# Kernel optimization log

Measured on AMD Instinct MI355X. Metric: run time of the kernel, lower is better.

## Reference

```python
import jax, jax.numpy as jnp
import numpy as np

HIDDEN = 96
INF = 1e30


def setup_inputs() -> dict:
    key = jax.random.key(0)
    ks = jax.random.split(key, 9)
    B, JX, JM, D_IN, D_MEM = 8, 2048, 2048, 150, 150
    GATED = D_IN + D_MEM  # 300
    inputs = jax.random.normal(ks[0], (B, JX, D_IN), dtype=jnp.float32)
    memory = jax.random.normal(ks[1], (B, JM, D_MEM), dtype=jnp.float32)
    mask = jax.random.randint(ks[2], (B, JM), 0, 2, dtype=jnp.int32)
    s_in = 1.0 / np.sqrt(D_IN)
    s_g = 1.0 / np.sqrt(GATED)
    Wi = jax.random.uniform(ks[3], (D_IN, HIDDEN), jnp.float32, -s_in, s_in)
    bi = jax.random.uniform(ks[4], (HIDDEN,), jnp.float32, -s_in, s_in)
    Wm = jax.random.uniform(ks[5], (D_MEM, HIDDEN), jnp.float32, -s_in, s_in)
    bm = jax.random.uniform(ks[6], (HIDDEN,), jnp.float32, -s_in, s_in)
    Wg = jax.random.uniform(ks[7], (GATED, GATED), jnp.float32, -s_g, s_g)
    bg = jax.random.uniform(ks[8], (GATED,), jnp.float32, -s_g, s_g)
    return {"inputs": inputs, "memory": memory, "mask": mask,
            "Wi": Wi, "bi": bi, "Wm": Wm, "bm": bm, "Wg": Wg, "bg": bg}


def reference(inputs, memory, mask, Wi, bi, Wm, bm, Wg, bg):
    # ReLU projections (inference mode: dropout is identity)
    inputs_ = jax.nn.relu(jnp.einsum('bxd,dh->bxh', inputs, Wi) + bi)  # [B,JX,H]
    memory_ = jax.nn.relu(jnp.einsum('byd,dh->byh', memory, Wm) + bm)  # [B,JM,H]
    # Scaled dot-product scores [B,JX,JM]
    scores = jnp.einsum('bxh,byh->bxy', inputs_, memory_) / jnp.sqrt(
        jnp.asarray(HIDDEN, inputs.dtype))
    # Additive mask: -INF where mask==0 (broadcast over JX)
    maskf = mask.astype(inputs.dtype)[:, None, :]  # [B,1,JM]
    scores = scores - INF * (1.0 - maskf)
    logits = jax.nn.softmax(scores, axis=-1)
    outputs = jnp.einsum('bxy,byd->bxd', logits, memory)  # [B,JX,D_MEM]
    res = jnp.concatenate([inputs, outputs], axis=2)  # [B,JX,GATED]
    gate = jax.nn.sigmoid(jnp.einsum('bxg,gk->bxk', res, Wg) + bg)
    return gate * res
```

## Files before the change

### kernel.cpp

```cpp
#include <hip/hip_runtime.h>

#define BB 8
#define JX 2048
#define JMDIM 2048
#define DID 150
#define HID 96
#define GATED 300
#define NSPLIT 4
#define NROWS (BB * JX)

typedef unsigned short u16;
typedef __attribute__((ext_vector_type(8))) short bh8;
typedef __attribute__((ext_vector_type(4))) float f32x4;

#define SCALE2    (0.14724444f)
#define MASK_NEG2 (-1.4426950e30f)

__device__ inline float b2f(u16 u) {
    union { unsigned int i; float f; } c; c.i = ((unsigned int)u) << 16; return c.f;
}
__device__ inline u16 f2b(float f) {
    unsigned int u = __float_as_uint(f);
    unsigned int r = (u + 0x7fffu + ((u >> 16) & 1u)) >> 16;
    return (u16)r;
}

__global__ void prep_kernel(const float* __restrict__ Wi, const float* __restrict__ Wm,
                            const float* __restrict__ Wg,
                            u16* __restrict__ Wti, u16* __restrict__ Wtm,
                            u16* __restrict__ Wgt) {
    int tid = blockIdx.x * blockDim.x + threadIdx.x;
    int nthr = gridDim.x * blockDim.x;
    for (int e = tid; e < 96 * 168; e += nthr) {
        int h = e / 168, d = e - h * 168;
        Wti[e] = (d < DID) ? f2b(Wi[d * HID + h]) : (u16)0;
        Wtm[e] = (d < DID) ? f2b(Wm[d * HID + h]) : (u16)0;
    }
    for (int e = tid; e < 304 * 328; e += nthr) {
        int k = e / 328, d = e - k * 328;
        Wgt[e] = (k < GATED && d < GATED) ? f2b(Wg[d * GATED + k]) : (u16)0;
    }
}

__global__ __launch_bounds__(256) void proj2_kernel(
    const float* __restrict__ inputs, const float* __restrict__ memory,
    const u16* __restrict__ Wti, const u16* __restrict__ Wtm,
    const float* __restrict__ bi, const float* __restrict__ bm,
    u16* __restrict__ Qp, u16* __restrict__ Kp,
    u16* __restrict__ Xi, u16* __restrict__ Vt) {
    __shared__ __align__(16) u16 Xl[64 * 168];
    __shared__ __align__(16) u16 Wl[96 * 168];
    const float *X, *bias; const u16* Wt; u16* Y;
    if (blockIdx.y == 0) { X = inputs; Wt = Wti; bias = bi; Y = Qp; }
    else                 { X = memory; Wt = Wtm; bias = bm; Y = Kp; }
    int tid = threadIdx.x;
    size_t row0 = (size_t)blockIdx.x * 64;

    const float4* Xv = (const float4*)(X + row0 * DID);
    for (int i = tid; i < 2400; i += 256) {
        float4 v = Xv[i];
        int base = i * 4;
#pragma unroll
        for (int k = 0; k < 4; ++k) {
            int idx = base + k;
            int r = idx / DID, d = idx - r * DID;
            Xl[r * 168 + d] = f2b(((const float*)&v)[k]);
        }
    }
    for (int e = tid; e < 64 * 18; e += 256) {
        int r = e / 18, d = 150 + (e - r * 18);
        Xl[r * 168 + d] = 0;
    }
    for (int i = tid; i < 96 * 21; i += 256) {
        *(bh8*)(Wl + i * 8) = *(const bh8*)(Wt + i * 8);
    }
    __syncthreads();

    if (blockIdx.y == 0) {
        for (int e = tid; e < 64 * 20; e += 256) {
            int r = e / 20, c = e - r * 20;
            *(bh8*)(Xi + (row0 + r) * 160 + c * 8) = *(const bh8*)(Xl + r * 168 + c * 8);
        }
    } else {
        int b = blockIdx.x >> 5, jm0 = (blockIdx.x & 31) * 64;
        for (int e = tid; e < 160 * 64; e += 256) {
            int d = e >> 6, c = e & 63;
            u16 v = (d == DID) ? (u16)0x3F80 : Xl[c * 168 + d];
            Vt[((size_t)b * 160 + d) * JMDIM + jm0 + c] = v;
        }
    }

    int wave = tid >> 6, lane = tid & 63, quad = lane >> 4, l15 = lane & 15;
    bh8 af[5];
#pragma unroll
    for (int kc = 0; kc < 5; ++kc)
        af[kc] = *(const bh8*)(Xl + (wave * 16 + l15) * 168 + kc * 32 + quad * 8);
#pragma unroll
    for (int nt = 0; nt < 6; ++nt) {
        f32x4 acc = {0.f, 0.f, 0.f, 0.f};
#pragma unroll
        for (int kc = 0; kc < 5; ++kc) {
            bh8 bf = *(const bh8*)(Wl + (nt * 16 + l15) * 168 + kc * 32 + quad * 8);
            acc = __builtin_amdgcn_mfma_f32_16x16x32_bf16(af[kc], bf, acc, 0, 0, 0);
        }
        int h = nt * 16 + l15;
        float bv = bias[h];
#pragma unroll
        for (int j = 0; j < 4; ++j) {
            float y = acc[j] + bv;
            y = y > 0.f ? y : 0.f;
            Y[(row0 + wave * 16 + quad * 4 + j) * HID + h] = f2b(y);
        }
    }
}

template <int SPLIT>
__global__ __launch_bounds__(256, 2) void attn_kernel(
    const u16* __restrict__ Qp, const u16* __restrict__ Kp,
    const u16* __restrict__ Vt, const int* __restrict__ mask,
    u16* __restrict__ Opart, float* __restrict__ lpart) {
    __shared__ __align__(16) u16 Kl[64 * 104];
    __shared__ __align__(16) u16 Vl[160 * 72];
    __shared__ __align__(16) u16 Pl[128 * 72];
    __shared__ float Ml[64];
    const int b = blockIdx.y;
    const int x0 = blockIdx.x * 128;
    const int tid = threadIdx.x;
    const int wave = tid >> 6, lane = tid & 63;
    const int quad = lane >> 4, l15 = lane & 15;

    bh8 qf[2][3];
#pragma unroll
    for (int mt = 0; mt < 2; ++mt) {
        const u16* qb = Qp + ((size_t)b * JX + x0 + wave * 32 + mt * 16 + l15) * HID + quad * 8;
        qf[mt][0] = *(const bh8*)(qb);
        qf[mt][1] = *(const bh8*)(qb + 32);
        qf[mt][2] = *(const bh8*)(qb + 64);
    }

    f32x4 o[2][10];
    const f32x4 zero4 = {0.f, 0.f, 0.f, 0.f};
#pragma unroll
    for (int mt = 0; mt < 2; ++mt)
#pragma unroll
        for (int i = 0; i < 10; ++i) o[mt][i] = zero4;

    const int nIter = 32 / SPLIT;
    const int jm0_0 = blockIdx.z * nIter * 64;

    const u16* kptr[3]; u16* kdst[3];
#pragma unroll
    for (int t = 0; t < 3; ++t) {
        int i = tid + t * 256, r = i / 12, c = i - r * 12;
        kptr[t] = Kp + ((size_t)b * JMDIM + jm0_0 + r) * HID + c * 8;
        kdst[t] = Kl + r * 104 + c * 8;
    }
    const u16* vptr[5]; u16* vdst[5];
#pragma unroll
    for (int t = 0; t < 5; ++t) {
        int i = tid + t * 256, d = i >> 3, c = i & 7;
        vptr[t] = Vt + ((size_t)b * 160 + d) * JMDIM + jm0_0 + c * 8;
        vdst[t] = Vl + d * 72 + c * 8;
    }
    const int* mptr = mask + b * JMDIM + jm0_0 + (tid & 63);

    bh8 kreg[3], vreg[5]; int mreg = 0;
#pragma unroll
    for (int t = 0; t < 3; ++t) { kreg[t] = *(const bh8*)kptr[t]; kptr[t] += 64 * HID; }
#pragma unroll
    for (int t = 0; t < 5; ++t) { vreg[t] = *(const bh8*)vptr[t]; vptr[t] += 64; }
    if (tid < 64) { mreg = *mptr; mptr += 64; }

    for (int it = 0; it < nIter; ++it) {
        __syncthreads();
#pragma unroll
        for (int t = 0; t < 3; ++t) *(bh8*)kdst[t] = kreg[t];
#pragma unroll
        for (int t = 0; t < 5; ++t) *(bh8*)vdst[t] = vreg[t];
        if (tid < 64) Ml[tid] = mreg ? 0.f : MASK_NEG2;
        if (it + 1 < nIter) {
#pragma unroll
            for (int t = 0; t < 3; ++t) { kreg[t] = *(const bh8*)kptr[t]; kptr[t] += 64 * HID; }
#pragma unroll
            for (int t = 0; t < 5; ++t) { vreg[t] = *(const bh8*)vptr[t]; vptr[t] += 64; }
            if (tid < 64) { mreg = *mptr; mptr += 64; }
        }
        __syncthreads();

        f32x4 s[2][4];
#pragma unroll
        for (int mt = 0; mt < 2; ++mt)
#pragma unroll
            for (int nt = 0; nt < 4; ++nt) s[mt][nt] = zero4;
#pragma unroll
        for (int nt = 0; nt < 4; ++nt) {
#pragma unroll
            for (int kc = 0; kc < 3; ++kc) {
                bh8 bf = *(const bh8*)(Kl + (nt * 16 + l15) * 104 + kc * 32 + quad * 8);
                s[0][nt] = __builtin_amdgcn_mfma_f32_16x16x32_bf16(qf[0][kc], bf, s[0][nt], 0, 0, 0);
                s[1][nt] = __builtin_amdgcn_mfma_f32_16x16x32_bf16(qf[1][kc], bf, s[1][nt], 0, 0, 0);
            }
        }
#pragma unroll
        for (int nt = 0; nt < 4; ++nt) {
            float madd = Ml[nt * 16 + l15];
#pragma unroll
            for (int mt = 0; mt < 2; ++mt)
#pragma unroll
                for (int j = 0; j < 4; ++j) {
                    float p = exp2f(s[mt][nt][j] * SCALE2 + madd);
                    Pl[(wave * 32 + mt * 16 + quad * 4 + j) * 72 + nt * 16 + l15] = f2b(p);
                }
        }
        __threadfence_block();

        bh8 pf[2][2];
#pragma unroll
        for (int mt = 0; mt < 2; ++mt) {
            pf[mt][0] = *(const bh8*)(Pl + (wave * 32 + mt * 16 + l15) * 72 + quad * 8);
            pf[mt][1] = *(const bh8*)(Pl + (wave * 32 + mt * 16 + l15) * 72 + 32 + quad * 8);
        }
#pragma unroll
        for (int nt = 0; nt < 10; ++nt) {
#pragma unroll
            for (int kc = 0; kc < 2; ++kc) {
                bh8 bf = *(const bh8*)(Vl + (nt * 16 + l15) * 72 + kc * 32 + quad * 8);
                o[0][nt] = __builtin_amdgcn_mfma_f32_16x16x32_bf16(pf[0][kc], bf, o[0][nt], 0, 0, 0);
                o[1][nt] = __builtin_amdgcn_mfma_f32_16x16x32_bf16(pf[1][kc], bf, o[1][nt], 0, 0, 0);
            }
        }
    }

    const size_t z = blockIdx.z;
    const int srcLane = (lane & 48) | 6;
#pragma unroll
    for (int mt = 0; mt < 2; ++mt) {
        float lv[4], inv[4];
#pragma unroll
        for (int j = 0; j < 4; ++j) {
            lv[j] = __shfl(o[mt][9][j], srcLane, 64);
            inv[j] = (lv[j] > 0.f) ? 1.f / lv[j] : 0.f;
        }
        size_t grow = (size_t)b * JX + x0 + wave * 32 + mt * 16;
#pragma unroll
        for (int nt = 0; nt < 10; ++nt) {
            int d = nt * 16 + l15;
            if (d < 152) {
#pragma unroll
                for (int j = 0; j < 4; ++j)
                    Opart[(z * NROWS + grow + quad * 4 + j) * 152 + d] = f2b(o[mt][nt][j] * inv[j]);
            }
        }
        if (l15 == 0) {
#pragma unroll
            for (int j = 0; j < 4; ++j)
                lpart[z * NROWS + grow + quad * 4 + j] = lv[j];
        }
    }
}

template <int SPLIT>
__global__ __launch_bounds__(256) void gate_kernel(
    const u16* __restrict__ Xi, const u16* __restrict__ Opart,
    const float* __restrict__ lpart,
    const u16* __restrict__ Wgt, const float* __restrict__ bg,
    float* __restrict__ out) {
    __shared__ __align__(16) u16 Rl[16 * 328];
    __shared__ float Cw[SPLIT * 16];
    int tid = threadIdx.x;
    size_t row0 = (size_t)blockIdx.x * 16;

    if (tid < 16) {
        float l[SPLIT], L = 0.f;
#pragma unroll
        for (int s = 0; s < SPLIT; ++s) {
            l[s] = lpart[(size_t)s * NROWS + row0 + tid];
            L += l[s];
        }
        float invL = (L > 0.f) ? 1.f / L : 0.f;
#pragma unroll
        for (int s = 0; s < SPLIT; ++s) Cw[s * 16 + tid] = l[s] * invL;
    }
    for (int e = tid; e < 16 * 20; e += 256) {
        int r = e / 20, c = e - r * 20;
        *(bh8*)(Rl + r * 328 + c * 8) = *(const bh8*)(Xi + (row0 + r) * 160 + c * 8);
    }
    __syncthreads();
    for (int e = tid; e < 16 * 19; e += 256) {
        int r = e / 19, q = e - r * 19;
        float acc[8];
#pragma unroll
        for (int k = 0; k < 8; ++k) acc[k] = 0.f;
#pragma unroll
        for (int s = 0; s < SPLIT; ++s) {
            bh8 v = *(const bh8*)(Opart + ((size_t)s * NROWS + row0 + r) * 152 + q * 8);
            float w = Cw[s * 16 + r];
#pragma unroll
            for (int k = 0; k < 8; ++k) acc[k] += b2f(((const u16*)&v)[k]) * w;
        }
        u16* dst = Rl + r * 328 + 150 + q * 8;
#pragma unroll
        for (int k = 0; k < 8; ++k) dst[k] = f2b(acc[k]);
    }
    for (int e = tid; e < 16 * 26; e += 256) {
        int r = e / 26, c = 302 + (e - r * 26);
        Rl[r * 328 + c] = 0;
    }
    __syncthreads();

    int wave = tid >> 6, lane = tid & 63, quad = lane >> 4, l15 = lane & 15;
    bh8 af[10];
#pragma unroll
    for (int kc = 0; kc < 10; ++kc)
        af[kc] = *(const bh8*)(Rl + l15 * 328 + kc * 32 + quad * 8);
    for (int nt = wave; nt < 19; nt += 4) {
        int h = nt * 16 + l15;
        f32x4 acc = {0.f, 0.f, 0.f, 0.f};
#pragma unroll
        for (int kc = 0; kc < 10; ++kc) {
            bh8 bf = *(const bh8*)(Wgt + (size_t)h * 328 + kc * 32 + quad * 8);
            acc = __builtin_amdgcn_mfma_f32_16x16x32_bf16(af[kc], bf, acc, 0, 0, 0);
        }
        if (h < GATED) {
            float bv = bg[h];
#pragma unroll
            for (int j = 0; j < 4; ++j) {
                int r = quad * 4 + j;
                float x = acc[j] + bv;
                float g = 1.f / (1.f + __expf(-x));
                float rv = b2f(Rl[r * 328 + h]);
                out[(row0 + r) * GATED + h] = g * rv;
            }
        }
    }
}

extern "C" void kernel_launch(void* const* d_in, const int* in_sizes, int n_in,
                              void* d_out, int out_size, void* d_ws, size_t ws_size,
                              hipStream_t stream) {
    const float* inputs = (const float*)d_in[0];
    const float* memory = (const float*)d_in[1];
    const int*   mask   = (const int*)d_in[2];
    const float* Wi = (const float*)d_in[3];
    const float* bi = (const float*)d_in[4];
    const float* Wm = (const float*)d_in[5];
    const float* bm = (const float*)d_in[6];
    const float* Wg = (const float*)d_in[7];
    const float* bg = (const float*)d_in[8];
    float* out = (float*)d_out;

    u16* Qp  = (u16*)d_ws;
    u16* Kp  = Qp + (size_t)NROWS * HID;
    u16* Vt  = Kp + (size_t)NROWS * HID;
    u16* Xi  = Vt + (size_t)BB * 160 * JMDIM;
    u16* Wti = Xi + (size_t)NROWS * 160;
    u16* Wtm = Wti + 96 * 168;
    u16* Wgt = Wtm + 96 * 168;
    u16* Opart = Wgt + 304 * 328;
    size_t u16_elems = (size_t)(Opart - Qp) + (size_t)NSPLIT * NROWS * 152;
    size_t base_bytes = ((u16_elems * sizeof(u16)) + 15) & ~(size_t)15;
    float* lpart = (float*)((char*)d_ws + base_bytes);
    size_t needed = base_bytes + (size_t)NSPLIT * NROWS * sizeof(float);
    if (ws_size < needed) return;

    prep_kernel<<<dim3(128), 256, 0, stream>>>(Wi, Wm, Wg, Wti, Wtm, Wgt);
    proj2_kernel<<<dim3(NROWS / 64, 2), 256, 0, stream>>>(
        inputs, memory, Wti, Wtm, bi, bm, Qp, Kp, Xi, Vt);
    attn_kernel<NSPLIT><<<dim3(JX / 128, BB, NSPLIT), 256, 0, stream>>>(
        Qp, Kp, Vt, mask, Opart, lpart);
    gate_kernel<NSPLIT><<<dim3(NROWS / 16), 256, 0, stream>>>(
        Xi, Opart, lpart, Wgt, bg, out);
}
```

Before: 144.0 us.

## Double attention query tile to 256 rows, raise split to 8, widen gate tile

Each attention block now handles 256 query rows (64 per wave) so every K/V tile staged in shared memory feeds twice as many rows. The JM split is raised to 8 to keep the grid size the same. Q fragments are reloaded from global memory per pair inside the loop instead of being held in registers, and the register double-buffered K/V prefetch is replaced by a load-then-store each iteration. The gate kernel processes 32 rows per block so each Wg fragment is reused across two MFMA row tiles. The costs are more accumulator registers, less load/compute overlap, repeated Q reads, and twice the partial output traffic for the gate merge.

```diff
diff --git a/kernel.cpp b/kernel.cpp
--- a/kernel.cpp
+++ b/kernel.cpp
@@ -6,7 +6,7 @@
 #define DID 150
 #define HID 96
 #define GATED 300
-#define NSPLIT 4
+#define NSPLIT 8
 #define NROWS (BB * JX)
 
 typedef unsigned short u16;
@@ -121,112 +121,112 @@
     u16* __restrict__ Opart, float* __restrict__ lpart) {
     __shared__ __align__(16) u16 Kl[64 * 104];
     __shared__ __align__(16) u16 Vl[160 * 72];
-    __shared__ __align__(16) u16 Pl[128 * 72];
+    __shared__ __align__(16) u16 Pl[256 * 72];
     __shared__ float Ml[64];
     const int b = blockIdx.y;
-    const int x0 = blockIdx.x * 128;
+    const int x0 = blockIdx.x * 256;
     const int tid = threadIdx.x;
     const int wave = tid >> 6, lane = tid & 63;
     const int quad = lane >> 4, l15 = lane & 15;
 
-    bh8 qf[2][3];
-#pragma unroll
-    for (int mt = 0; mt < 2; ++mt) {
-        const u16* qb = Qp + ((size_t)b * JX + x0 + wave * 32 + mt * 16 + l15) * HID + quad * 8;
-        qf[mt][0] = *(const bh8*)(qb);
-        qf[mt][1] = *(const bh8*)(qb + 32);
-        qf[mt][2] = *(const bh8*)(qb + 64);
-    }
-
-    f32x4 o[2][10];
+    f32x4 o[4][10];
     const f32x4 zero4 = {0.f, 0.f, 0.f, 0.f};
 #pragma unroll
-    for (int mt = 0; mt < 2; ++mt)
+    for (int mt = 0; mt < 4; ++mt)
 #pragma unroll
         for (int i = 0; i < 10; ++i) o[mt][i] = zero4;
 
     const int nIter = 32 / SPLIT;
     const int jm0_0 = blockIdx.z * nIter * 64;
 
-    const u16* kptr[3]; u16* kdst[3];
+    int koff[3]; u16* kdst[3];
 #pragma unroll
     for (int t = 0; t < 3; ++t) {
         int i = tid + t * 256, r = i / 12, c = i - r * 12;
-        kptr[t] = Kp + ((size_t)b * JMDIM + jm0_0 + r) * HID + c * 8;
+        koff[t] = r * HID + c * 8;
         kdst[t] = Kl + r * 104 + c * 8;
     }
-    const u16* vptr[5]; u16* vdst[5];
+    int voff[5]; u16* vdst[5];
 #pragma unroll
     for (int t = 0; t < 5; ++t) {
         int i = tid + t * 256, d = i >> 3, c = i & 7;
-        vptr[t] = Vt + ((size_t)b * 160 + d) * JMDIM + jm0_0 + c * 8;
+        voff[t] = d * JMDIM + c * 8;
         vdst[t] = Vl + d * 72 + c * 8;
     }
-    const int* mptr = mask + b * JMDIM + jm0_0 + (tid & 63);
-
-    bh8 kreg[3], vreg[5]; int mreg = 0;
-#pragma unroll
-    for (int t = 0; t < 3; ++t) { kreg[t] = *(const bh8*)kptr[t]; kptr[t] += 64 * HID; }
-#pragma unroll
-    for (int t = 0; t < 5; ++t) { vreg[t] = *(const bh8*)vptr[t]; vptr[t] += 64; }
-    if (tid < 64) { mreg = *mptr; mptr += 64; }
+    const u16* kbase = Kp + ((size_t)b * JMDIM + jm0_0) * HID;
+    const u16* vbase = Vt + (size_t)b * 160 * JMDIM + jm0_0;
+    const int* mbase = mask + b * JMDIM + jm0_0 + (tid & 63);
+    const u16* qrow = Qp + ((size_t)b * JX + x0 + wave * 64 + l15) * HID + quad * 8;
 
     for (int it = 0; it < nIter; ++it) {
+        bh8 kt[3], vt[5]; int mreg = 0;
+#pragma unroll
+        for (int t = 0; t < 3; ++t) kt[t] = *(const bh8*)(kbase + koff[t]);
+#pragma unroll
+        for (int t = 0; t < 5; ++t) vt[t] = *(const bh8*)(vbase + voff[t]);
+        if (tid < 64) mreg = mbase[0];
         __syncthreads();
 #pragma unroll
-        for (int t = 0; t < 3; ++t) *(bh8*)kdst[t] = kreg[t];
-#pragma unroll
-        for (int t = 0; t < 5; ++t) *(bh8*)vdst[t] = vreg[t];
+        for (int t = 0; t < 3; ++t) *(bh8*)kdst[t] = kt[t];
+#pragma unroll
+        for (int t = 0; t < 5; ++t) *(bh8*)vdst[t] = vt[t];
         if (tid < 64) Ml[tid] = mreg ? 0.f : MASK_NEG2;
-        if (it + 1 < nIter) {
-#pragma unroll
-            for (int t = 0; t < 3; ++t) { kreg[t] = *(const bh8*)kptr[t]; kptr[t] += 64 * HID; }
-#pragma unroll
-            for (int t = 0; t < 5; ++t) { vreg[t] = *(const bh8*)vptr[t]; vptr[t] += 64; }
-            if (tid < 64) { mreg = *mptr; mptr += 64; }
-        }
+        kbase += 64 * HID; vbase += 64; mbase += 64;
         __syncthreads();
 
-        f32x4 s[2][4];
-#pragma unroll
-        for (int mt = 0; mt < 2; ++mt)
-#pragma unroll
-            for (int nt = 0; nt < 4; ++nt) s[mt][nt] = zero4;
-#pragma unroll
-        for (int nt = 0; nt < 4; ++nt) {
-#pragma unroll
-            for (int kc = 0; kc < 3; ++kc) {
-                bh8 bf = *(const bh8*)(Kl + (nt * 16 + l15) * 104 + kc * 32 + quad * 8);
-                s[0][nt] = __builtin_amdgcn_mfma_f32_16x16x32_bf16(qf[0][kc], bf, s[0][nt], 0, 0, 0);
-                s[1][nt] = __builtin_amdgcn_mfma_f32_16x16x32_bf16(qf[1][kc], bf, s[1][nt], 0, 0, 0);
-            }
-        }
-#pragma unroll
-        for (int nt = 0; nt < 4; ++nt) {
-            float madd = Ml[nt * 16 + l15];
-#pragma unroll
-            for (int mt = 0; mt < 2; ++mt)
-#pragma unroll
-                for (int j = 0; j < 4; ++j) {
-                    float p = exp2f(s[mt][nt][j] * SCALE2 + madd);
-                    Pl[(wave * 32 + mt * 16 + quad * 4 + j) * 72 + nt * 16 + l15] = f2b(p);
+#pragma unroll
+        for (int pair = 0; pair < 2; ++pair) {
+            bh8 qf[2][3];
+#pragma unroll
+            for (int m2 = 0; m2 < 2; ++m2) {
+                const u16* qb = qrow + (size_t)(pair * 2 + m2) * 16 * HID;
+                qf[m2][0] = *(const bh8*)(qb);
+                qf[m2][1] = *(const bh8*)(qb + 32);
+                qf[m2][2] = *(const bh8*)(qb + 64);
+            }
+            f32x4 s[2][4];
+#pragma unroll
+            for (int m2 = 0; m2 < 2; ++m2)
+#pragma unroll
+                for (int nt = 0; nt < 4; ++nt) s[m2][nt] = zero4;
+#pragma unroll
+            for (int nt = 0; nt < 4; ++nt) {
+#pragma unroll
+                for (int kc = 0; kc < 3; ++kc) {
+                    bh8 bf = *(const bh8*)(Kl + (nt * 16 + l15) * 104 + kc * 32 + quad * 8);
+                    s[0][nt] = __builtin_amdgcn_mfma_f32_16x16x32_bf16(qf[0][kc], bf, s[0][nt], 0, 0, 0);
+                    s[1][nt] = __builtin_amdgcn_mfma_f32_16x16x32_bf16(qf[1][kc], bf, s[1][nt], 0, 0, 0);
                 }
+            }
+#pragma unroll
+            for (int nt = 0; nt < 4; ++nt) {
+                float madd = Ml[nt * 16 + l15];
+#pragma unroll
+                for (int m2 = 0; m2 < 2; ++m2)
+#pragma unroll
+                    for (int j = 0; j < 4; ++j) {
+                        float p = exp2f(s[m2][nt][j] * SCALE2 + madd);
+                        Pl[(wave * 64 + (pair * 2 + m2) * 16 + quad * 4 + j) * 72
+                           + nt * 16 + l15] = f2b(p);
+                    }
+            }
         }
         __threadfence_block();
 
-        bh8 pf[2][2];
-#pragma unroll
-        for (int mt = 0; mt < 2; ++mt) {
-            pf[mt][0] = *(const bh8*)(Pl + (wave * 32 + mt * 16 + l15) * 72 + quad * 8);
-            pf[mt][1] = *(const bh8*)(Pl + (wave * 32 + mt * 16 + l15) * 72 + 32 + quad * 8);
+        bh8 pf[4][2];
+#pragma unroll
+        for (int mt = 0; mt < 4; ++mt) {
+            pf[mt][0] = *(const bh8*)(Pl + (wave * 64 + mt * 16 + l15) * 72 + quad * 8);
+            pf[mt][1] = *(const bh8*)(Pl + (wave * 64 + mt * 16 + l15) * 72 + 32 + quad * 8);
         }
 #pragma unroll
         for (int nt = 0; nt < 10; ++nt) {
 #pragma unroll
             for (int kc = 0; kc < 2; ++kc) {
                 bh8 bf = *(const bh8*)(Vl + (nt * 16 + l15) * 72 + kc * 32 + quad * 8);
-                o[0][nt] = __builtin_amdgcn_mfma_f32_16x16x32_bf16(pf[0][kc], bf, o[0][nt], 0, 0, 0);
-                o[1][nt] = __builtin_amdgcn_mfma_f32_16x16x32_bf16(pf[1][kc], bf, o[1][nt], 0, 0, 0);
+#pragma unroll
+                for (int mt = 0; mt < 4; ++mt)
+                    o[mt][nt] = __builtin_amdgcn_mfma_f32_16x16x32_bf16(pf[mt][kc], bf, o[mt][nt], 0, 0, 0);
             }
         }
     }
@@ -234,14 +234,14 @@
     const size_t z = blockIdx.z;
     const int srcLane = (lane & 48) | 6;
 #pragma unroll
-    for (int mt = 0; mt < 2; ++mt) {
+    for (int mt = 0; mt < 4; ++mt) {
         float lv[4], inv[4];
 #pragma unroll
         for (int j = 0; j < 4; ++j) {
             lv[j] = __shfl(o[mt][9][j], srcLane, 64);
             inv[j] = (lv[j] > 0.f) ? 1.f / lv[j] : 0.f;
         }
-        size_t grow = (size_t)b * JX + x0 + wave * 32 + mt * 16;
+        size_t grow = (size_t)b * JX + x0 + wave * 64 + mt * 16;
 #pragma unroll
         for (int nt = 0; nt < 10; ++nt) {
             int d = nt * 16 + l15;
@@ -265,12 +265,12 @@
     const float* __restrict__ lpart,
     const u16* __restrict__ Wgt, const float* __restrict__ bg,
     float* __restrict__ out) {
-    __shared__ __align__(16) u16 Rl[16 * 328];
-    __shared__ float Cw[SPLIT * 16];
+    __shared__ __align__(16) u16 Rl[32 * 328];
+    __shared__ float Cw[SPLIT * 32];
     int tid = threadIdx.x;
-    size_t row0 = (size_t)blockIdx.x * 16;
-
-    if (tid < 16) {
+    size_t row0 = (size_t)blockIdx.x * 32;
+
+    if (tid < 32) {
         float l[SPLIT], L = 0.f;
 #pragma unroll
         for (int s = 0; s < SPLIT; ++s) {
@@ -279,14 +279,14 @@
         }
         float invL = (L > 0.f) ? 1.f / L : 0.f;
 #pragma unroll
-        for (int s = 0; s < SPLIT; ++s) Cw[s * 16 + tid] = l[s] * invL;
-    }
-    for (int e = tid; e < 16 * 20; e += 256) {
+        for (int s = 0; s < SPLIT; ++s) Cw[s * 32 + tid] = l[s] * invL;
+    }
+    for (int e = tid; e < 32 * 20; e += 256) {
         int r = e / 20, c = e - r * 20;
         *(bh8*)(Rl + r * 328 + c * 8) = *(const bh8*)(Xi + (row0 + r) * 160 + c * 8);
     }
     __syncthreads();
-    for (int e = tid; e < 16 * 19; e += 256) {
+    for (int e = tid; e < 32 * 19; e += 256) {
         int r = e / 19, q = e - r * 19;
         float acc[8];
 #pragma unroll
@@ -294,7 +294,7 @@
 #pragma unroll
         for (int s = 0; s < SPLIT; ++s) {
             bh8 v = *(const bh8*)(Opart + ((size_t)s * NROWS + row0 + r) * 152 + q * 8);
-            float w = Cw[s * 16 + r];
+            float w = Cw[s * 32 + r];
 #pragma unroll
             for (int k = 0; k < 8; ++k) acc[k] += b2f(((const u16*)&v)[k]) * w;
         }
@@ -302,35 +302,41 @@
 #pragma unroll
         for (int k = 0; k < 8; ++k) dst[k] = f2b(acc[k]);
     }
-    for (int e = tid; e < 16 * 26; e += 256) {
+    for (int e = tid; e < 32 * 26; e += 256) {
         int r = e / 26, c = 302 + (e - r * 26);
         Rl[r * 328 + c] = 0;
     }
     __syncthreads();
 
     int wave = tid >> 6, lane = tid & 63, quad = lane >> 4, l15 = lane & 15;
-    bh8 af[10];
-#pragma unroll
-    for (int kc = 0; kc < 10; ++kc)
-        af[kc] = *(const bh8*)(Rl + l15 * 328 + kc * 32 + quad * 8);
+    bh8 af[2][10];
+#pragma unroll
+    for (int rh = 0; rh < 2; ++rh)
+#pragma unroll
+        for (int kc = 0; kc < 10; ++kc)
+            af[rh][kc] = *(const bh8*)(Rl + (rh * 16 + l15) * 328 + kc * 32 + quad * 8);
     for (int nt = wave; nt < 19; nt += 4) {
         int h = nt * 16 + l15;
-        f32x4 acc = {0.f, 0.f, 0.f, 0.f};
+        f32x4 acc0 = {0.f, 0.f, 0.f, 0.f};
+        f32x4 acc1 = {0.f, 0.f, 0.f, 0.f};
 #pragma unroll
         for (int kc = 0; kc < 10; ++kc) {
             bh8 bf = *(const bh8*)(Wgt + (size_t)h * 328 + kc * 32 + quad * 8);
-            acc = __builtin_amdgcn_mfma_f32_16x16x32_bf16(af[kc], bf, acc, 0, 0, 0);
+            acc0 = __builtin_amdgcn_mfma_f32_16x16x32_bf16(af[0][kc], bf, acc0, 0, 0, 0);
+            acc1 = __builtin_amdgcn_mfma_f32_16x16x32_bf16(af[1][kc], bf, acc1, 0, 0, 0);
         }
         if (h < GATED) {
             float bv = bg[h];
 #pragma unroll
-            for (int j = 0; j < 4; ++j) {
-                int r = quad * 4 + j;
-                float x = acc[j] + bv;
-                float g = 1.f / (1.f + __expf(-x));
-                float rv = b2f(Rl[r * 328 + h]);
-                out[(row0 + r) * GATED + h] = g * rv;
-            }
+            for (int rh = 0; rh < 2; ++rh)
+#pragma unroll
+                for (int j = 0; j < 4; ++j) {
+                    int r = rh * 16 + quad * 4 + j;
+                    float x = (rh ? acc1[j] : acc0[j]) + bv;
+                    float g = 1.f / (1.f + __expf(-x));
+                    float rv = b2f(Rl[r * 328 + h]);
+                    out[(row0 + r) * GATED + h] = g * rv;
+                }
         }
     }
 }
@@ -366,8 +372,8 @@
     prep_kernel<<<dim3(128), 256, 0, stream>>>(Wi, Wm, Wg, Wti, Wtm, Wgt);
     proj2_kernel<<<dim3(NROWS / 64, 2), 256, 0, stream>>>(
         inputs, memory, Wti, Wtm, bi, bm, Qp, Kp, Xi, Vt);
-    attn_kernel<NSPLIT><<<dim3(JX / 128, BB, NSPLIT), 256, 0, stream>>>(
+    attn_kernel<NSPLIT><<<dim3(JX / 256, BB, NSPLIT), 256, 0, stream>>>(
         Qp, Kp, Vt, mask, Opart, lpart);
-    gate_kernel<NSPLIT><<<dim3(NROWS / 16), 256, 0, stream>>>(
+    gate_kernel<NSPLIT><<<dim3(NROWS / 32), 256, 0, stream>>>(
         Xi, Opart, lpart, Wgt, bg, out);
 }
```

New measurement: 175.8 us. 22.1% more time.
